# Performance work log

Measured on AMD Instinct MI355X. Metric: run time of the kernel, lower is better.

The kernel has to match this reference:

```python
import jax, jax.numpy as jnp
import numpy as np

N = 100000
E = 3200000
D_IN = 256
D_OUT = 256
K = 3


def setup_inputs() -> dict:
    key = jax.random.key(0)
    k1, k2, k3, k4, k5 = jax.random.split(key, 5)
    x = jax.random.normal(k1, (N, D_IN), dtype=jnp.float32)
    # xavier-uniform-ish weight
    lim = float(np.sqrt(6.0 / (D_IN + D_OUT)))
    weight = jax.random.uniform(k2, (D_IN, D_OUT), dtype=jnp.float32, minval=-lim, maxval=lim)
    bias = jnp.zeros((D_OUT,), dtype=jnp.float32)
    edge_weight = jax.random.uniform(k3, (E,), dtype=jnp.float32) / 32.0  # ~normalized adj values
    edge_row = jax.random.randint(k4, (E,), 0, N, dtype=jnp.int32)
    edge_col = jax.random.randint(k5, (E,), 0, N, dtype=jnp.int32)
    return {"x": x, "weight": weight, "bias": bias, "edge_weight": edge_weight,
            "edge_row": edge_row, "edge_col": edge_col}


def _spmm(edge_weight, edge_row, edge_col, support):
    # out[i] = sum_{e: row_e == i} w_e * support[col_e]
    msgs = edge_weight[:, None] * support[edge_col]  # [E, D]
    return jax.ops.segment_sum(msgs, edge_row, num_segments=N)


def reference(x, weight, bias, edge_weight, edge_row, edge_col):
    support = x @ weight            # [N, D_OUT]
    output = support
    for _ in range(K):
        support = _spmm(edge_weight, edge_row, edge_col, support)
        output = output + support
    return output + bias
```

## Files before the change

### kernel.cpp

```cpp
#include <hip/hip_runtime.h>

#define D 256
#define NB 196
#define RPB_SHIFT 9
#define CAP 20480
#define CHUNK 8192
#define PADSLACK 4096

typedef __attribute__((ext_vector_type(8))) short bf16x8;
typedef __attribute__((ext_vector_type(4))) float f32x4;
typedef __attribute__((ext_vector_type(2))) float f32x2;

__device__ __forceinline__ unsigned bf16rne(float f) {
    unsigned u = __float_as_uint(f);
    return (u + 0x7fffu + ((u >> 16) & 1u)) >> 16;
}
__device__ __forceinline__ unsigned char fp8enc(float f) {
    return (unsigned char)(__builtin_amdgcn_cvt_pk_fp8_f32(f, f, 0, false) & 0xFF);
}


__global__ __launch_bounds__(256) void cursor_init(int* __restrict__ g) {
    int t = threadIdx.x;
    g[t] = t * CAP;
}

__global__ __launch_bounds__(256) void partA(const int* __restrict__ erow,
                                             const int* __restrict__ ecol,
                                             const float* __restrict__ ew,
                                             int* __restrict__ gcur,
                                             int2* __restrict__ temp, int E) {
    __shared__ int2 rec[CHUNK];
    __shared__ unsigned char bkt[CHUNK];
    __shared__ int hist[256], sc[256], excl[256], cur[256], lbase[256];
    int t = threadIdx.x;
    int base = blockIdx.x * CHUNK;
    hist[t] = 0;
    __syncthreads();
    int rows[32];
    #pragma unroll
    for (int j = 0; j < 32; j++) {
        int e = base + t + 256 * j;
        rows[j] = (e < E) ? erow[e] : -1;
        if (rows[j] >= 0) atomicAdd(&hist[rows[j] >> RPB_SHIFT], 1);
    }
    __syncthreads();
    sc[t] = hist[t];
    __syncthreads();
    for (int off = 1; off < 256; off <<= 1) {
        int v = (t >= off) ? sc[t - off] : 0;
        __syncthreads();
        sc[t] += v;
        __syncthreads();
    }
    int ex = sc[t] - hist[t];
    excl[t] = ex;
    cur[t] = ex;
    lbase[t] = atomicAdd(&gcur[t], hist[t]);
    __syncthreads();
    int total = sc[255];
    #pragma unroll
    for (int j = 0; j < 32; j++) {
        if (rows[j] >= 0) {
            int e = base + t + 256 * j;
            int b = rows[j] >> RPB_SHIFT;
            int rl = rows[j] & 511;
            int p = atomicAdd(&cur[b], 1);
            int2 r;
            r.x = ecol[e] | (rl << 17);
            r.y = __float_as_int(ew[e]);
            rec[p] = r;
            bkt[p] = (unsigned char)b;
        }
    }
    __syncthreads();
    for (int i = t; i < total; i += 256) {
        int b = bkt[i];
        temp[(size_t)lbase[b] + (i - excl[b])] = rec[i];
    }
}

__global__ __launch_bounds__(256) void scanB(const int* __restrict__ gcur,
                                             int* __restrict__ bbase) {
    __shared__ int sc[256];
    int t = threadIdx.x;
    int c = (t < NB) ? (gcur[t] - t * CAP) : 0;
    sc[t] = c;
    __syncthreads();
    for (int off = 1; off < 256; off <<= 1) {
        int v = (t >= off) ? sc[t - off] : 0;
        __syncthreads();
        sc[t] += v;
        __syncthreads();
    }
    if (t < NB) bbase[t] = sc[t] - c;
}

__global__ __launch_bounds__(256) void partB(const int2* __restrict__ temp,
                                             const int* __restrict__ gcur,
                                             const int* __restrict__ bbase,
                                             int* __restrict__ rps,
                                             int* __restrict__ rpe,
                                             int2* __restrict__ edges,
                                             int N, int E) {
    __shared__ int hist[512], excl[512], pst[512], scp[256];
    int b = blockIdx.x;
    int t = threadIdx.x;
    int cnt = gcur[b] - b * CAP;
    int base = bbase[b] + b * PADSLACK;
    const int2* src = temp + (size_t)b * CAP;
    hist[t] = 0;
    hist[t + 256] = 0;
    __syncthreads();
    for (int i = t; i < cnt; i += 256)
        atomicAdd(&hist[(src[i].x >> 17) & 511], 1);
    __syncthreads();
    int v0 = hist[2 * t], v1 = hist[2 * t + 1];
    int p0 = (v0 + 7) & ~7, p1 = (v1 + 7) & ~7;
    int ps = p0 + p1;
    scp[t] = ps;
    __syncthreads();
    for (int off = 1; off < 256; off <<= 1) {
        int v = (t >= off) ? scp[t - off] : 0;
        __syncthreads();
        scp[t] += v;
        __syncthreads();
    }
    int ep = scp[t] - ps;
    excl[2 * t] = ep;
    excl[2 * t + 1] = ep + p0;
    pst[2 * t] = ep;
    pst[2 * t + 1] = ep + p0;
    int r0 = (b << RPB_SHIFT) + 2 * t;
    if (r0 < N)     { rps[r0]     = base + ep;      rpe[r0]     = base + ep + p0; }
    if (r0 + 1 < N) { rps[r0 + 1] = base + ep + p0; rpe[r0 + 1] = base + ep + p0 + p1; }
    __syncthreads();
    for (int i = t; i < cnt; i += 256) {
        int2 r = src[i];
        int rl = (r.x >> 17) & 511;
        int p = base + atomicAdd(&excl[rl], 1);
        int2 o;
        o.x = (r.x & 0x1FFFF) << 8;
        o.y = r.y;
        edges[p] = o;
    }
    __syncthreads();
    int c0 = hist[2 * t];
    int b0 = base + pst[2 * t];
    for (int k = c0; k < p0; k++) edges[b0 + k] = make_int2(0, 0);
    int c1 = hist[2 * t + 1];
    int b1 = base + pst[2 * t + 1];
    for (int k = c1; k < p1; k++) edges[b1 + k] = make_int2(0, 0);
}

__global__ __launch_bounds__(256) void wconv_kernel(const float* __restrict__ w,
                                                    bf16x8* __restrict__ Wf) {
    int idx = blockIdx.x * 256 + threadIdx.x;
    int lane = idx & 63, g = idx >> 6;
    int h = g >> 6, r = g & 63;
    int ct = r >> 2, ks = (h << 2) | (r & 3);
    int q = lane >> 4, c = lane & 15;
    int n = ct * 16 + c;
    int k0 = ks * 32 + q * 8;
    bf16x8 bv;
    #pragma unroll
    for (int j = 0; j < 8; j++)
        bv[j] = (short)bf16rne(w[(size_t)(k0 + j) * D + n]);
    Wf[idx] = bv;
}

__global__ __launch_bounds__(512, 4) void gemm_kernel(const float* __restrict__ x,
                                                      const bf16x8* __restrict__ Wf,
                                                      const float* __restrict__ bias,
                                                      unsigned char* __restrict__ s0f8,
                                                      float* __restrict__ out, int N) {
    __shared__ bf16x8 Wl[4096];
    int t = threadIdx.x;
    int wid = t >> 6, lane = t & 63;
    int q = lane >> 4, c = lane & 15;
    int row0 = blockIdx.x * 128 + wid * 16;
    int rA = row0 + c;
    if (rA >= N) rA = N - 1;
    const float* xr = x + (size_t)rA * D + q * 8;

    f32x4 acc[16];
    #pragma unroll
    for (int ct = 0; ct < 16; ct++) acc[ct] = (f32x4){0.f, 0.f, 0.f, 0.f};

    for (int h = 0; h < 2; h++) {
        if (h) __syncthreads();
        #pragma unroll
        for (int k2 = 0; k2 < 8; k2++)
            Wl[k2 * 512 + t] = Wf[h * 4096 + k2 * 512 + t];
        __syncthreads();
        #pragma unroll
        for (int ks2 = 0; ks2 < 4; ks2++) {
            int ks = h * 4 + ks2;
            float4 p = *(const float4*)(xr + ks * 32);
            float4 r = *(const float4*)(xr + ks * 32 + 4);
            bf16x8 a;
            a[0] = (short)bf16rne(p.x); a[1] = (short)bf16rne(p.y);
            a[2] = (short)bf16rne(p.z); a[3] = (short)bf16rne(p.w);
            a[4] = (short)bf16rne(r.x); a[5] = (short)bf16rne(r.y);
            a[6] = (short)bf16rne(r.z); a[7] = (short)bf16rne(r.w);
            #pragma unroll
            for (int ct = 0; ct < 16; ct++) {
                bf16x8 bfrag = Wl[(ct * 4 + ks2) * 64 + lane];
                acc[ct] = __builtin_amdgcn_mfma_f32_16x16x32_bf16(a, bfrag, acc[ct], 0, 0, 0);
            }
        }
    }

    int rbase = row0 + q * 4;
    #pragma unroll
    for (int ct = 0; ct < 16; ct++) {
        int col = ct * 16 + c;
        float bv = bias[col];
        #pragma unroll
        for (int r = 0; r < 4; r++) {
            int rr = rbase + r;
            if (rr < N) {
                float v = acc[ct][r];
                size_t o = (size_t)rr * D + col;
                s0f8[o] = fp8enc(v);
                out[o] = v + bv;
            }
        }
    }
}

__global__ __launch_bounds__(256, 4) void spmm_kernel(const unsigned char* __restrict__ S,
                                                      const int* __restrict__ rps,
                                                      const int* __restrict__ rpe,
                                                      const int2* __restrict__ edges,
                                                      unsigned char* __restrict__ Snext, int N) {
    int t = threadIdx.x;
    int wid = t >> 6, lane = t & 63;
    int q = lane >> 4, ql = lane & 15;
    int row = blockIdx.x * 16 + wid * 4 + q;
    if (row >= N) return;
    int e   = rps[row];
    int end = rpe[row];
    const unsigned char* Sl = S + (ql << 4);

    f32x2 A[8];
    #pragma unroll
    for (int i = 0; i < 8; i++) A[i] = (f32x2){0.f, 0.f};

    int2 edn[8];
    #pragma unroll
    for (int j = 0; j < 8; j++) edn[j] = edges[e + j];

    while (e < end) {
        uint4 v[8];
        #pragma unroll
        for (int j = 0; j < 8; j++)
            v[j] = *(const uint4*)(Sl + (unsigned)edn[j].x);
        float w[8];
        #pragma unroll
        for (int j = 0; j < 8; j++) w[j] = __int_as_float(edn[j].y);
        #pragma unroll
        for (int j = 0; j < 8; j++) edn[j] = edges[e + 8 + j];
        #pragma unroll
        for (int j = 0; j < 8; j++) {
            f32x2 w2 = {w[j], w[j]};
            A[0] += w2 * __builtin_amdgcn_cvt_pk_f32_fp8(v[j].x, false);
            A[1] += w2 * __builtin_amdgcn_cvt_pk_f32_fp8(v[j].x, true);
            A[2] += w2 * __builtin_amdgcn_cvt_pk_f32_fp8(v[j].y, false);
            A[3] += w2 * __builtin_amdgcn_cvt_pk_f32_fp8(v[j].y, true);
            A[4] += w2 * __builtin_amdgcn_cvt_pk_f32_fp8(v[j].z, false);
            A[5] += w2 * __builtin_amdgcn_cvt_pk_f32_fp8(v[j].z, true);
            A[6] += w2 * __builtin_amdgcn_cvt_pk_f32_fp8(v[j].w, false);
            A[7] += w2 * __builtin_amdgcn_cvt_pk_f32_fp8(v[j].w, true);
        }
        e += 8;
    }
    unsigned s;
    uint4 o;
    s   = (unsigned)__builtin_amdgcn_cvt_pk_fp8_f32(A[0].x, A[0].y, 0, false);
    o.x = (unsigned)__builtin_amdgcn_cvt_pk_fp8_f32(A[1].x, A[1].y, (int)s, true);
    s   = (unsigned)__builtin_amdgcn_cvt_pk_fp8_f32(A[2].x, A[2].y, 0, false);
    o.y = (unsigned)__builtin_amdgcn_cvt_pk_fp8_f32(A[3].x, A[3].y, (int)s, true);
    s   = (unsigned)__builtin_amdgcn_cvt_pk_fp8_f32(A[4].x, A[4].y, 0, false);
    o.z = (unsigned)__builtin_amdgcn_cvt_pk_fp8_f32(A[5].x, A[5].y, (int)s, true);
    s   = (unsigned)__builtin_amdgcn_cvt_pk_fp8_f32(A[6].x, A[6].y, 0, false);
    o.w = (unsigned)__builtin_amdgcn_cvt_pk_fp8_f32(A[7].x, A[7].y, (int)s, true);
    *(uint4*)(Snext + (size_t)row * 256 + (ql << 4)) = o;
}

__global__ __launch_bounds__(256, 4) void spmm_fused_kernel(const unsigned char* __restrict__ S,
                                                            const int* __restrict__ rps,
                                                            const int* __restrict__ rpe,
                                                            const int2* __restrict__ edges,
                                                            const unsigned char* __restrict__ S1,
                                                            float* __restrict__ out, int N) {
    int t = threadIdx.x;
    int wid = t >> 6, lane = t & 63;
    int q = lane >> 4, ql = lane & 15;
    int row = blockIdx.x * 16 + wid * 4 + q;
    if (row >= N) return;
    int e   = rps[row];
    int end = rpe[row];
    const unsigned char* Sl = S + (ql << 4);

    f32x2 A[8];
    #pragma unroll
    for (int i = 0; i < 8; i++) A[i] = (f32x2){0.f, 0.f};

    int2 edn[8];
    #pragma unroll
    for (int j = 0; j < 8; j++) edn[j] = edges[e + j];

    while (e < end) {
        uint4 v[8];
        #pragma unroll
        for (int j = 0; j < 8; j++)
            v[j] = *(const uint4*)(Sl + (unsigned)edn[j].x);
        float w[8];
        #pragma unroll
        for (int j = 0; j < 8; j++) w[j] = __int_as_float(edn[j].y);
        #pragma unroll
        for (int j = 0; j < 8; j++) edn[j] = edges[e + 8 + j];
        #pragma unroll
        for (int j = 0; j < 8; j++) {
            f32x2 w2 = {w[j], w[j]};
            A[0] += w2 * __builtin_amdgcn_cvt_pk_f32_fp8(v[j].x, false);
            A[1] += w2 * __builtin_amdgcn_cvt_pk_f32_fp8(v[j].x, true);
            A[2] += w2 * __builtin_amdgcn_cvt_pk_f32_fp8(v[j].y, false);
            A[3] += w2 * __builtin_amdgcn_cvt_pk_f32_fp8(v[j].y, true);
            A[4] += w2 * __builtin_amdgcn_cvt_pk_f32_fp8(v[j].z, false);
            A[5] += w2 * __builtin_amdgcn_cvt_pk_f32_fp8(v[j].z, true);
            A[6] += w2 * __builtin_amdgcn_cvt_pk_f32_fp8(v[j].w, false);
            A[7] += w2 * __builtin_amdgcn_cvt_pk_f32_fp8(v[j].w, true);
        }
        e += 8;
    }
    size_t rb = (size_t)row * 256 + (ql << 4);
    uint4 u1 = *(const uint4*)(S1 + rb);
    uint4 u2 = *(const uint4*)(S + rb);
    A[0] += __builtin_amdgcn_cvt_pk_f32_fp8(u1.x, false) + __builtin_amdgcn_cvt_pk_f32_fp8(u2.x, false);
    A[1] += __builtin_amdgcn_cvt_pk_f32_fp8(u1.x, true)  + __builtin_amdgcn_cvt_pk_f32_fp8(u2.x, true);
    A[2] += __builtin_amdgcn_cvt_pk_f32_fp8(u1.y, false) + __builtin_amdgcn_cvt_pk_f32_fp8(u2.y, false);
    A[3] += __builtin_amdgcn_cvt_pk_f32_fp8(u1.y, true)  + __builtin_amdgcn_cvt_pk_f32_fp8(u2.y, true);
    A[4] += __builtin_amdgcn_cvt_pk_f32_fp8(u1.z, false) + __builtin_amdgcn_cvt_pk_f32_fp8(u2.z, false);
    A[5] += __builtin_amdgcn_cvt_pk_f32_fp8(u1.z, true)  + __builtin_amdgcn_cvt_pk_f32_fp8(u2.z, true);
    A[6] += __builtin_amdgcn_cvt_pk_f32_fp8(u1.w, false) + __builtin_amdgcn_cvt_pk_f32_fp8(u2.w, false);
    A[7] += __builtin_amdgcn_cvt_pk_f32_fp8(u1.w, true)  + __builtin_amdgcn_cvt_pk_f32_fp8(u2.w, true);
    float* op = out + (size_t)row * 256 + (ql << 4);
    #pragma unroll
    for (int k = 0; k < 4; k++) {
        float4 o = *(const float4*)(op + 4 * k);
        o.x += A[2 * k].x;
        o.y += A[2 * k].y;
        o.z += A[2 * k + 1].x;
        o.w += A[2 * k + 1].y;
        *(float4*)(op + 4 * k) = o;
    }
}

extern "C" void kernel_launch(void* const* d_in, const int* in_sizes, int n_in,
                              void* d_out, int out_size, void* d_ws, size_t ws_size,
                              hipStream_t stream) {
    const float* x      = (const float*)d_in[0];
    const float* weight = (const float*)d_in[1];
    const float* bias   = (const float*)d_in[2];
    const float* ew     = (const float*)d_in[3];
    const int*   erow   = (const int*)d_in[4];
    const int*   ecol   = (const int*)d_in[5];
    float* out = (float*)d_out;
    int N = in_sizes[0] / D;
    int E = in_sizes[3];

    char* ws = (char*)d_ws;
    size_t off = 0;
    auto walloc = [&](size_t bytes) -> void* {
        void* p = ws + off;
        off += (bytes + 255) & ~255ULL;
        return p;
    };
    unsigned char* Sa = (unsigned char*)walloc((size_t)N * D);
    unsigned char* Sb = (unsigned char*)walloc((size_t)N * D);
    unsigned char* Sc = (unsigned char*)walloc((size_t)N * D);
    int*    rps     = (int*)walloc((size_t)N * 4);
    int*    rpe     = (int*)walloc((size_t)N * 4);
    int*    gcur    = (int*)walloc(256 * 4);
    int*    bbase   = (int*)walloc(256 * 4);
    bf16x8* Wf      = (bf16x8*)walloc(128 * 64 * 16);
    int2*   temp    = (int2*)walloc((size_t)NB * CAP * 8);
    int2*   edges   = (int2*)walloc(((size_t)E + (size_t)NB * PADSLACK + 64) * 8);

    cursor_init<<<1, 256, 0, stream>>>(gcur);
    int nchunks = (E + CHUNK - 1) / CHUNK;
    partA<<<nchunks, 256, 0, stream>>>(erow, ecol, ew, gcur, temp, E);
    scanB<<<1, 256, 0, stream>>>(gcur, bbase);
    partB<<<NB, 256, 0, stream>>>(temp, gcur, bbase, rps, rpe, edges, N, E);

    wconv_kernel<<<32, 256, 0, stream>>>(weight, Wf);
    gemm_kernel<<<(N + 127) / 128, 512, 0, stream>>>(x, Wf, bias, Sa, out, N);

    int sb = (N + 15) / 16;
    spmm_kernel<<<sb, 256, 0, stream>>>(Sa, rps, rpe, edges, Sb, N);
    spmm_kernel<<<sb, 256, 0, stream>>>(Sb, rps, rpe, edges, Sc, N);
    spmm_fused_kernel<<<sb, 256, 0, stream>>>(Sc, rps, rpe, edges, Sb, out, N);
}
```

Baseline: 694.8 us.

## Replace bucketed two-pass CSR build with global atomic count-scan-scatter

Replaces the LDS-based two-level bucket partition (partA/scanB/partB) with a simple CSR build. It counts per-row degrees with global atomics, runs a single-block scan that pads each row to a multiple of 8, and scatters edges with per-row atomic cursors, zero-filling the padding. This drops the temp buffer and the staged shared-memory sorting. In exchange it issues millions of random global atomics and uncoalesced 8-byte writes, and the scan runs serially per thread in one block. Edge order within a row also becomes nondeterministic.

```diff
diff --git a/kernel.cpp b/kernel.cpp
--- a/kernel.cpp
+++ b/kernel.cpp
@@ -1,11 +1,6 @@
 #include <hip/hip_runtime.h>
 
 #define D 256
-#define NB 196
-#define RPB_SHIFT 9
-#define CAP 20480
-#define CHUNK 8192
-#define PADSLACK 4096
 
 typedef __attribute__((ext_vector_type(8))) short bf16x8;
 typedef __attribute__((ext_vector_type(4))) float f32x4;
@@ -20,137 +15,89 @@
 }
 
 
-__global__ __launch_bounds__(256) void cursor_init(int* __restrict__ g) {
+__global__ __launch_bounds__(256) void zero_cnt(int* __restrict__ rowcnt, int N) {
+    int i = blockIdx.x * 256 + threadIdx.x;
+    if (i < N) rowcnt[i] = 0;
+}
+
+__global__ __launch_bounds__(256) void count_k(const int* __restrict__ erow,
+                                               int* __restrict__ rowcnt, int E) {
+    int gid = blockIdx.x * 256 + threadIdx.x;
+    int e0 = gid * 4;
+    if (e0 + 3 < E) {
+        int4 r4 = *(const int4*)(erow + e0);
+        atomicAdd(&rowcnt[r4.x], 1);
+        atomicAdd(&rowcnt[r4.y], 1);
+        atomicAdd(&rowcnt[r4.z], 1);
+        atomicAdd(&rowcnt[r4.w], 1);
+    } else {
+        for (int e = e0; e < E; e++) atomicAdd(&rowcnt[erow[e]], 1);
+    }
+}
+
+__global__ __launch_bounds__(1024) void scan_k(const int* __restrict__ rowcnt,
+                                               int* __restrict__ rps,
+                                               int* __restrict__ rpe,
+                                               int* __restrict__ cursor, int N) {
+    __shared__ int ts[1024];
     int t = threadIdx.x;
-    g[t] = t * CAP;
-}
-
-__global__ __launch_bounds__(256) void partA(const int* __restrict__ erow,
-                                             const int* __restrict__ ecol,
-                                             const float* __restrict__ ew,
-                                             int* __restrict__ gcur,
-                                             int2* __restrict__ temp, int E) {
-    __shared__ int2 rec[CHUNK];
-    __shared__ unsigned char bkt[CHUNK];
-    __shared__ int hist[256], sc[256], excl[256], cur[256], lbase[256];
-    int t = threadIdx.x;
-    int base = blockIdx.x * CHUNK;
-    hist[t] = 0;
+    int per = (N + 1023) / 1024;
+    int lo = t * per;
+    int hi = lo + per < N ? lo + per : N;
+    int sum = 0;
+    for (int r = lo; r < hi; r++) sum += (rowcnt[r] + 7) & ~7;
+    ts[t] = sum;
     __syncthreads();
-    int rows[32];
-    #pragma unroll
-    for (int j = 0; j < 32; j++) {
-        int e = base + t + 256 * j;
-        rows[j] = (e < E) ? erow[e] : -1;
-        if (rows[j] >= 0) atomicAdd(&hist[rows[j] >> RPB_SHIFT], 1);
-    }
-    __syncthreads();
-    sc[t] = hist[t];
-    __syncthreads();
-    for (int off = 1; off < 256; off <<= 1) {
-        int v = (t >= off) ? sc[t - off] : 0;
+    for (int off = 1; off < 1024; off <<= 1) {
+        int v = (t >= off) ? ts[t - off] : 0;
         __syncthreads();
-        sc[t] += v;
+        ts[t] += v;
         __syncthreads();
     }
-    int ex = sc[t] - hist[t];
-    excl[t] = ex;
-    cur[t] = ex;
-    lbase[t] = atomicAdd(&gcur[t], hist[t]);
-    __syncthreads();
-    int total = sc[255];
-    #pragma unroll
-    for (int j = 0; j < 32; j++) {
-        if (rows[j] >= 0) {
-            int e = base + t + 256 * j;
-            int b = rows[j] >> RPB_SHIFT;
-            int rl = rows[j] & 511;
-            int p = atomicAdd(&cur[b], 1);
-            int2 r;
-            r.x = ecol[e] | (rl << 17);
-            r.y = __float_as_int(ew[e]);
-            rec[p] = r;
-            bkt[p] = (unsigned char)b;
-        }
-    }
-    __syncthreads();
-    for (int i = t; i < total; i += 256) {
-        int b = bkt[i];
-        temp[(size_t)lbase[b] + (i - excl[b])] = rec[i];
-    }
-}
-
-__global__ __launch_bounds__(256) void scanB(const int* __restrict__ gcur,
-                                             int* __restrict__ bbase) {
-    __shared__ int sc[256];
-    int t = threadIdx.x;
-    int c = (t < NB) ? (gcur[t] - t * CAP) : 0;
-    sc[t] = c;
-    __syncthreads();
-    for (int off = 1; off < 256; off <<= 1) {
-        int v = (t >= off) ? sc[t - off] : 0;
-        __syncthreads();
-        sc[t] += v;
-        __syncthreads();
-    }
-    if (t < NB) bbase[t] = sc[t] - c;
-}
-
-__global__ __launch_bounds__(256) void partB(const int2* __restrict__ temp,
-                                             const int* __restrict__ gcur,
-                                             const int* __restrict__ bbase,
-                                             int* __restrict__ rps,
-                                             int* __restrict__ rpe,
-                                             int2* __restrict__ edges,
-                                             int N, int E) {
-    __shared__ int hist[512], excl[512], pst[512], scp[256];
-    int b = blockIdx.x;
-    int t = threadIdx.x;
-    int cnt = gcur[b] - b * CAP;
-    int base = bbase[b] + b * PADSLACK;
-    const int2* src = temp + (size_t)b * CAP;
-    hist[t] = 0;
-    hist[t + 256] = 0;
-    __syncthreads();
-    for (int i = t; i < cnt; i += 256)
-        atomicAdd(&hist[(src[i].x >> 17) & 511], 1);
-    __syncthreads();
-    int v0 = hist[2 * t], v1 = hist[2 * t + 1];
-    int p0 = (v0 + 7) & ~7, p1 = (v1 + 7) & ~7;
-    int ps = p0 + p1;
-    scp[t] = ps;
-    __syncthreads();
-    for (int off = 1; off < 256; off <<= 1) {
-        int v = (t >= off) ? scp[t - off] : 0;
-        __syncthreads();
-        scp[t] += v;
-        __syncthreads();
-    }
-    int ep = scp[t] - ps;
-    excl[2 * t] = ep;
-    excl[2 * t + 1] = ep + p0;
-    pst[2 * t] = ep;
-    pst[2 * t + 1] = ep + p0;
-    int r0 = (b << RPB_SHIFT) + 2 * t;
-    if (r0 < N)     { rps[r0]     = base + ep;      rpe[r0]     = base + ep + p0; }
-    if (r0 + 1 < N) { rps[r0 + 1] = base + ep + p0; rpe[r0 + 1] = base + ep + p0 + p1; }
-    __syncthreads();
-    for (int i = t; i < cnt; i += 256) {
-        int2 r = src[i];
-        int rl = (r.x >> 17) & 511;
-        int p = base + atomicAdd(&excl[rl], 1);
-        int2 o;
-        o.x = (r.x & 0x1FFFF) << 8;
-        o.y = r.y;
-        edges[p] = o;
-    }
-    __syncthreads();
-    int c0 = hist[2 * t];
-    int b0 = base + pst[2 * t];
-    for (int k = c0; k < p0; k++) edges[b0 + k] = make_int2(0, 0);
-    int c1 = hist[2 * t + 1];
-    int b1 = base + pst[2 * t + 1];
-    for (int k = c1; k < p1; k++) edges[b1 + k] = make_int2(0, 0);
+    int run = ts[t] - sum;
+    for (int r = lo; r < hi; r++) {
+        int c = rowcnt[r];
+        int p = (c + 7) & ~7;
+        rps[r] = run;
+        cursor[r] = run;
+        rpe[r] = run + p;
+        run += p;
+    }
+}
+
+__global__ __launch_bounds__(256) void scatter_k(const int* __restrict__ erow,
+                                                 const int* __restrict__ ecol,
+                                                 const float* __restrict__ ew,
+                                                 int* __restrict__ cursor,
+                                                 const int* __restrict__ rowcnt,
+                                                 const int* __restrict__ rps,
+                                                 const int* __restrict__ rpe,
+                                                 int2* __restrict__ edges, int E, int N) {
+    int gid = blockIdx.x * 256 + threadIdx.x;
+    int e0 = gid * 4;
+    if (e0 + 3 < E) {
+        int4 r4 = *(const int4*)(erow + e0);
+        int4 c4 = *(const int4*)(ecol + e0);
+        float4 w4 = *(const float4*)(ew + e0);
+        int p0 = atomicAdd(&cursor[r4.x], 1);
+        int p1 = atomicAdd(&cursor[r4.y], 1);
+        int p2 = atomicAdd(&cursor[r4.z], 1);
+        int p3 = atomicAdd(&cursor[r4.w], 1);
+        edges[p0] = make_int2(c4.x << 8, __float_as_int(w4.x));
+        edges[p1] = make_int2(c4.y << 8, __float_as_int(w4.y));
+        edges[p2] = make_int2(c4.z << 8, __float_as_int(w4.z));
+        edges[p3] = make_int2(c4.w << 8, __float_as_int(w4.w));
+    } else {
+        for (int e = e0; e < E; e++) {
+            int p = atomicAdd(&cursor[erow[e]], 1);
+            edges[p] = make_int2(ecol[e] << 8, __float_as_int(ew[e]));
+        }
+    }
+    if (gid < N) {
+        int s = rps[gid] + rowcnt[gid];
+        int pe2 = rpe[gid];
+        for (int k = s; k < pe2; k++) edges[k] = make_int2(0, 0);
+    }
 }
 
 __global__ __launch_bounds__(256) void wconv_kernel(const float* __restrict__ w,
@@ -383,17 +330,18 @@
     unsigned char* Sc = (unsigned char*)walloc((size_t)N * D);
     int*    rps     = (int*)walloc((size_t)N * 4);
     int*    rpe     = (int*)walloc((size_t)N * 4);
-    int*    gcur    = (int*)walloc(256 * 4);
-    int*    bbase   = (int*)walloc(256 * 4);
+    int*    rowcnt  = (int*)walloc((size_t)N * 4);
+    int*    cursor  = (int*)walloc((size_t)N * 4);
     bf16x8* Wf      = (bf16x8*)walloc(128 * 64 * 16);
-    int2*   temp    = (int2*)walloc((size_t)NB * CAP * 8);
-    int2*   edges   = (int2*)walloc(((size_t)E + (size_t)NB * PADSLACK + 64) * 8);
-
-    cursor_init<<<1, 256, 0, stream>>>(gcur);
-    int nchunks = (E + CHUNK - 1) / CHUNK;
-    partA<<<nchunks, 256, 0, stream>>>(erow, ecol, ew, gcur, temp, E);
-    scanB<<<1, 256, 0, stream>>>(gcur, bbase);
-    partB<<<NB, 256, 0, stream>>>(temp, gcur, bbase, rps, rpe, edges, N, E);
+    int2*   edges   = (int2*)walloc(((size_t)E + (size_t)N * 7 + 64) * 8);
+
+    int nb1 = (N + 255) / 256;
+    int nb4 = (E + 1023) / 1024;
+    zero_cnt<<<nb1, 256, 0, stream>>>(rowcnt, N);
+    count_k<<<nb4, 256, 0, stream>>>(erow, rowcnt, E);
+    scan_k<<<1, 1024, 0, stream>>>(rowcnt, rps, rpe, cursor, N);
+    scatter_k<<<nb4, 256, 0, stream>>>(erow, ecol, ew, cursor, rowcnt, rps, rpe,
+                                       edges, E, N);
 
     wconv_kernel<<<32, 256, 0, stream>>>(weight, Wf);
     gemm_kernel<<<(N + 127) / 128, 512, 0, stream>>>(x, Wf, bias, Sa, out, N);
```

Measured after the change: 1.219 ms. 1.75x slower.
